# Optimization experiments

Hardware: AMD Instinct MI355X
Metric: run time of the kernel (lower is better)

## Reference

```python
import jax, jax.numpy as jnp
import numpy as np

N_NODES = 100000
N_EDGES = 1250000
IN_CH, HID_CH, OUT_CH = 128, 64, 40


def setup_inputs() -> dict:
    key = jax.random.key(0)
    ks = jax.random.split(key, 8)
    x = jax.random.normal(ks[0], (N_NODES, IN_CH), dtype=jnp.float32)
    edge_index = jax.random.randint(ks[1], (2, N_EDGES), 0, N_NODES, dtype=jnp.int64)
    # Glorot-ish scaled weights
    W1 = jax.random.normal(ks[2], (IN_CH, HID_CH), dtype=jnp.float32) * (1.0 / np.sqrt(IN_CH))
    b1 = jnp.zeros((HID_CH,), dtype=jnp.float32)
    W2 = jax.random.normal(ks[3], (HID_CH, HID_CH), dtype=jnp.float32) * (1.0 / np.sqrt(HID_CH))
    b2 = jnp.zeros((HID_CH,), dtype=jnp.float32)
    W3 = jax.random.normal(ks[4], (HID_CH, OUT_CH), dtype=jnp.float32) * (1.0 / np.sqrt(HID_CH))
    b3 = jnp.zeros((OUT_CH,), dtype=jnp.float32)
    return {"x": x, "edge_index": edge_index, "W1": W1, "b1": b1,
            "W2": W2, "b2": b2, "W3": W3, "b3": b3}


def reference(x, edge_index, W1, b1, W2, b2, W3, b3):
    n = x.shape[0]
    # PyG GCNConv: add self-loops, symmetric deg^-1/2 normalization
    loop = jnp.arange(n, dtype=edge_index.dtype)
    src = jnp.concatenate([edge_index[0], loop])  # [E+N]
    dst = jnp.concatenate([edge_index[1], loop])
    deg = jax.ops.segment_sum(jnp.ones_like(dst, dtype=x.dtype), dst, num_segments=n)
    dinv = jnp.where(deg > 0, jax.lax.rsqrt(deg), 0.0)
    coef = (dinv[src] * dinv[dst])[:, None]  # [E+N, 1]

    def conv(h, W, b):
        h = h @ W                                  # [N, F_out]
        msg = h[src] * coef                        # gather + scale: [E+N, F_out]
        return jax.ops.segment_sum(msg, dst, num_segments=n) + b

    h = jax.nn.relu(conv(x, W1, b1))   # dropout is identity in eval mode
    h = jax.nn.relu(conv(h, W2, b2))
    h = conv(h, W3, b3)
    return jax.nn.log_softmax(h, axis=1)
```

## Files before the change

### kernel.cpp

```cpp
#include <hip/hip_runtime.h>
#include <hip/hip_fp16.h>

#define NN 100000
#define NE 1250000
#define NBIN 512
#define RBIN 196
#define PAD 16
#define CAP 4096
#define EPB 4096
#define EPT 16

__device__ __forceinline__ int eidx(const int* __restrict__ e32, int f, int i){
    return f ? e32[2*(size_t)i] : e32[i];
}

__device__ __forceinline__ void scan_bins(const int* __restrict__ binCnt, int* __restrict__ boff){
    if(threadIdx.x < 64){
        int b0 = threadIdx.x*8;
        int pre[8]; int run = 0;
        #pragma unroll
        for(int i = 0; i < 8; ++i){ pre[i] = run; run += binCnt[(b0+i)*PAD]; }
        int inc = run;
        for(int o = 1; o < 64; o <<= 1){
            int u = __shfl_up(inc, o, 64);
            if(threadIdx.x >= (unsigned)o) inc += u;
        }
        int excl = inc - run;
        #pragma unroll
        for(int i = 0; i < 8; ++i) boff[b0+i] = excl + pre[i];
    }
    __syncthreads();
}

__global__ __launch_bounds__(256) void binA_k(const int* __restrict__ e32, int* __restrict__ binCnt){
    __shared__ int h[NBIN];
    __shared__ int flg;
    for(int t = threadIdx.x; t < NBIN; t += 256) h[t] = 0;
    if(threadIdx.x < 64){
        int v = e32[2*threadIdx.x + 1];
        unsigned long long b = __ballot(v != 0);
        if(threadIdx.x == 0) flg = (b == 0ULL) ? 1 : 0;
    }
    __syncthreads();
    const int f = flg;
    int base = blockIdx.x * 2048;
    #pragma unroll
    for(int k = 0; k < 8; ++k){
        int i = base + k*256 + threadIdx.x;
        if(i < NE){
            int d = eidx(e32, f, NE + i);
            atomicAdd(&h[d / RBIN], 1);
        }
    }
    __syncthreads();
    for(int t = threadIdx.x; t < NBIN; t += 256){
        int v = h[t];
        if(v) atomicAdd(&binCnt[t*PAD], v);
    }
}

__global__ __launch_bounds__(256) void binC_k(const int* __restrict__ e32, const int* __restrict__ binCnt,
                                              int* __restrict__ binCur, int2* __restrict__ bins){
    __shared__ int2 ST[EPB];
    __shared__ int hist[NBIN];
    __shared__ int lstart[NBIN];
    __shared__ int gbase[NBIN];
    __shared__ int cur[NBIN];
    __shared__ int boff[NBIN];
    __shared__ int flg;
    const int t = threadIdx.x;
    const int e0 = blockIdx.x * EPB;
    const int n = min(EPB, NE - e0);

    for(int b = t; b < NBIN; b += 256){ hist[b] = 0; cur[b] = 0; }
    if(t < 64){
        int v = e32[2*t + 1];
        unsigned long long b = __ballot(v != 0);
        if(t == 0) flg = (b == 0ULL) ? 1 : 0;
    }
    __syncthreads();
    const int f = flg;
    scan_bins(binCnt, boff);

    int2 ed[EPT];
    #pragma unroll
    for(int k = 0; k < EPT; ++k){
        int i = k*256 + t;
        if(i < n){
            ed[k].x = eidx(e32, f, e0 + i);
            ed[k].y = eidx(e32, f, NE + e0 + i);
            atomicAdd(&hist[ed[k].y / RBIN], 1);
        }
    }
    __syncthreads();

    if(t < 64){
        int b0 = t*8;
        int pre[8]; int run = 0;
        #pragma unroll
        for(int i = 0; i < 8; ++i){ pre[i] = run; run += hist[b0 + i]; }
        int inc = run;
        for(int o = 1; o < 64; o <<= 1){
            int u = __shfl_up(inc, o, 64);
            if(t >= o) inc += u;
        }
        int excl = inc - run;
        #pragma unroll
        for(int i = 0; i < 8; ++i) lstart[b0 + i] = excl + pre[i];
    }
    for(int b = t; b < NBIN; b += 256) gbase[b] = boff[b] + atomicAdd(&binCur[b*PAD], hist[b]);
    __syncthreads();

    #pragma unroll
    for(int k = 0; k < EPT; ++k){
        int i = k*256 + t;
        if(i < n){
            int b = ed[k].y / RBIN;
            int lo = atomicAdd(&cur[b], 1);
            ST[lstart[b] + lo] = ed[k];
        }
    }
    __syncthreads();

    for(int i = t; i < n; i += 256){
        int2 e = ST[i];
        int b = e.y / RBIN;
        bins[gbase[b] + (i - lstart[b])] = e;
    }
}

__global__ __launch_bounds__(256) void binD_k(const int2* __restrict__ bins, const int* __restrict__ binCnt,
                                              int* __restrict__ rp, float* __restrict__ dinv,
                                              int* __restrict__ csr_src){
    __shared__ int2 ES[CAP];
    __shared__ int hist[256];
    __shared__ int sc[256];
    __shared__ int cur[256];
    __shared__ int boff[NBIN];
    const int b = blockIdx.x;
    const int t = threadIdx.x;
    if(b == NBIN-1 && t == 0) rp[NN] = NE;
    const int nbase = b * RBIN;
    if(nbase >= NN) return;
    const int nend = min(nbase + RBIN, NN);
    const int nr = nend - nbase;
    hist[t] = 0; cur[t] = 0;
    __syncthreads();
    scan_bins(binCnt, boff);
    const int off0 = boff[b];
    const int cnt  = binCnt[b*PAD];

    const bool single = (cnt <= CAP);
    for(int c0 = 0; c0 < cnt; c0 += CAP){
        int n = min(CAP, cnt - c0);
        for(int i = t; i < n; i += 256) ES[i] = bins[off0 + c0 + i];
        __syncthreads();
        for(int i = t; i < n; i += 256) atomicAdd(&hist[ES[i].y - nbase], 1);
        __syncthreads();
    }
    int v = hist[t];
    sc[t] = v; __syncthreads();
    for(int off = 1; off < 256; off <<= 1){
        int u = (t >= off) ? sc[t - off] : 0;
        __syncthreads();
        sc[t] += u;
        __syncthreads();
    }
    int excl = sc[t] - v;
    sc[t] = excl;
    if(t < nr){
        rp[nbase + t]   = off0 + excl;
        dinv[nbase + t] = rsqrtf((float)(v + 1));
    }
    __syncthreads();
    for(int c0 = 0; c0 < cnt; c0 += CAP){
        int n = min(CAP, cnt - c0);
        if(!single){
            for(int i = t; i < n; i += 256) ES[i] = bins[off0 + c0 + i];
            __syncthreads();
        }
        for(int i = t; i < n; i += 256){
            int dl = ES[i].y - nbase;
            int p = atomicAdd(&cur[dl], 1);
            csr_src[off0 + sc[dl] + p] = ES[i].x;
        }
        if(!single) __syncthreads();
    }
}

template<int K, int NC, int KT, bool RELU>
__global__ __launch_bounds__(256) void gemm_k(const float* __restrict__ A, const float* __restrict__ W,
                                              const float* __restrict__ dinv,
                                              __half* __restrict__ out, int M){
    constexpr int CHT = KT/4;
    constexpr int CMASK = CHT - 1;
    __shared__ float Xs[64*KT];
    __shared__ float Ws[KT*NC];
    const int tid  = threadIdx.x;
    const int base = blockIdx.x * 64;
    const int tx = tid & 15, ty = tid >> 4;
    const int c0 = tx * 4;
    float acc[4][4] = {};

    for(int k0 = 0; k0 < K; k0 += KT){
        {
            const float4* Wv = (const float4*)(W + k0*NC);
            float4* Wsv = (float4*)Ws;
            for(int i = tid; i < KT*NC/4; i += 256) Wsv[i] = Wv[i];
        }
        {
            const int ch = tid & (CHT - 1);
            const int r0 = tid / CHT;
            constexpr int RSTEP = 256 / CHT;
            #pragma unroll
            for(int r = r0; r < 64; r += RSTEP){
                int row = base + r; if(row >= M) row = M - 1;
                float4 v = *(const float4*)&A[(size_t)row*K + k0 + ch*4];
                if(RELU){ v.x=fmaxf(v.x,0.f); v.y=fmaxf(v.y,0.f); v.z=fmaxf(v.z,0.f); v.w=fmaxf(v.w,0.f); }
                int sw = (ch + r) & CMASK;
                *(float4*)&Xs[r*KT + sw*4] = v;
            }
        }
        __syncthreads();

        if(c0 < NC){
            for(int k4 = 0; k4 < CHT; ++k4){
                float4 xs[4];
                #pragma unroll
                for(int i = 0; i < 4; ++i){
                    int r = ty*4 + i;
                    int sw = (k4 + r) & CMASK;
                    xs[i] = *(const float4*)&Xs[r*KT + (sw << 2)];
                }
                float4 wsv[4];
                #pragma unroll
                for(int kk = 0; kk < 4; ++kk) wsv[kk] = *(const float4*)&Ws[(k4*4 + kk)*NC + c0];
                #pragma unroll
                for(int kk = 0; kk < 4; ++kk){
                    const float* wp = (const float*)&wsv[kk];
                    #pragma unroll
                    for(int i = 0; i < 4; ++i){
                        float xv = ((const float*)&xs[i])[kk];
                        #pragma unroll
                        for(int j = 0; j < 4; ++j) acc[i][j] += xv * wp[j];
                    }
                }
            }
        }
        __syncthreads();
    }
    #pragma unroll
    for(int i = 0; i < 4; ++i){
        int row = base + ty*4 + i;
        if(row < M && c0 < NC){
            float dv = dinv[row];
            __half2 h01 = __floats2half2_rn(acc[i][0]*dv, acc[i][1]*dv);
            __half2 h23 = __floats2half2_rn(acc[i][2]*dv, acc[i][3]*dv);
            __half2* dst = (__half2*)&out[(size_t)row*NC + c0];
            dst[0] = h01;
            dst[1] = h23;
        }
    }
}

__global__ __launch_bounds__(256) void aggs_k(const __half* __restrict__ P, const int* __restrict__ rp,
                                              const int* __restrict__ csr_src,
                                              const float* __restrict__ dinv, const float* __restrict__ bias,
                                              float* __restrict__ G){
    const int lane = threadIdx.x & 63;
    const int idx  = (blockIdx.x*256 + threadIdx.x) >> 6;
    const int v    = idx >> 1;
    const int half = idx & 1;
    if(v >= NN) return;
    const int g = lane >> 3;
    const int q = lane & 7;
    const unsigned qo = (unsigned)(half*8 + q)*2;
    const __half2* __restrict__ P2 = (const __half2*)P;
    constexpr unsigned F2 = 32;

    const int beg = rp[v], end = rp[v + 1];
    float4 acc = make_float4(0.f, 0.f, 0.f, 0.f);
    if(g == 0){
        __half2 a = P2[(unsigned)v*F2 + qo], b = P2[(unsigned)v*F2 + qo + 1];
        float2 fa = __half22float2(a), fb = __half22float2(b);
        acc = make_float4(fa.x, fa.y, fb.x, fb.y);
    }

    int j = beg;
    #pragma unroll 1
    for(; j + 16 <= end; j += 16){
        unsigned i0 = (unsigned)csr_src[j + g]    *F2 + qo;
        unsigned i1 = (unsigned)csr_src[j + 8 + g]*F2 + qo;
        __half2 a0 = P2[i0], b0 = P2[i0+1];
        __half2 a1 = P2[i1], b1 = P2[i1+1];
        __half2 sa = __hadd2(a0, a1), sb = __hadd2(b0, b1);
        float2 f0 = __half22float2(sa), f1 = __half22float2(sb);
        acc.x += f0.x; acc.y += f0.y; acc.z += f1.x; acc.w += f1.y;
    }
    if(j + 8 <= end){
        unsigned i0 = (unsigned)csr_src[j + g]*F2 + qo;
        __half2 a = P2[i0], b = P2[i0+1];
        float2 fa = __half22float2(a), fb = __half22float2(b);
        acc.x += fa.x; acc.y += fa.y; acc.z += fb.x; acc.w += fb.y;
        j += 8;
    }
    const int rem = end - j;
    if(g < rem){
        unsigned i0 = (unsigned)csr_src[j + g]*F2 + qo;
        __half2 a = P2[i0], b = P2[i0+1];
        float2 fa = __half22float2(a), fb = __half22float2(b);
        acc.x += fa.x; acc.y += fa.y; acc.z += fb.x; acc.w += fb.y;
    }

    #pragma unroll
    for(int m = 8; m <= 32; m <<= 1){
        acc.x += __shfl_xor(acc.x, m, 64);
        acc.y += __shfl_xor(acc.y, m, 64);
        acc.z += __shfl_xor(acc.z, m, 64);
        acc.w += __shfl_xor(acc.w, m, 64);
    }

    if(g == 0){
        const float d = dinv[v];
        float4 bb = *(const float4*)&bias[half*32 + q*4];
        float4 r;
        r.x = fmaf(acc.x, d, bb.x);
        r.y = fmaf(acc.y, d, bb.y);
        r.z = fmaf(acc.z, d, bb.z);
        r.w = fmaf(acc.w, d, bb.w);
        *(float4*)&G[(size_t)v*64 + half*32 + q*4] = r;
    }
}

__global__ __launch_bounds__(256) void agg40_k(const __half* __restrict__ P, const int* __restrict__ rp,
                                               const int* __restrict__ csr_src,
                                               const float* __restrict__ dinv, const float* __restrict__ bias,
                                               float* __restrict__ G){
    constexpr int F = 40;
    constexpr int NQ = 10;
    constexpr unsigned F2 = 20;
    const int lane = threadIdx.x & 63;
    const int v = (blockIdx.x*256 + threadIdx.x) >> 6;
    if(v >= NN) return;
    const int g = lane >> 4;
    const int q = lane & 15;
    const bool qa = (q < NQ);
    const unsigned qo = (unsigned)q*2;
    const __half2* __restrict__ P2 = (const __half2*)P;

    const int beg = rp[v], end = rp[v + 1];
    float4 acc = make_float4(0.f, 0.f, 0.f, 0.f);
    if(g == 0 && qa){
        __half2 a = P2[(unsigned)v*F2 + qo], b = P2[(unsigned)v*F2 + qo + 1];
        float2 fa = __half22float2(a), fb = __half22float2(b);
        acc = make_float4(fa.x, fa.y, fb.x, fb.y);
    }

    int j = beg;
    #pragma unroll 1
    for(; j + 8 <= end; j += 8){
        unsigned i0 = (unsigned)csr_src[j + g]    *F2 + qo;
        unsigned i1 = (unsigned)csr_src[j + 4 + g]*F2 + qo;
        __half2 a0 = P2[i0], b0 = P2[i0+1];
        __half2 a1 = P2[i1], b1 = P2[i1+1];
        __half2 sa = __hadd2(a0, a1), sb = __hadd2(b0, b1);
        float2 f0 = __half22float2(sa), f1 = __half22float2(sb);
        acc.x += f0.x; acc.y += f0.y; acc.z += f1.x; acc.w += f1.y;
    }
    if(j + 4 <= end){
        unsigned i0 = (unsigned)csr_src[j + g]*F2 + qo;
        __half2 a = P2[i0], b = P2[i0+1];
        float2 fa = __half22float2(a), fb = __half22float2(b);
        acc.x += fa.x; acc.y += fa.y; acc.z += fb.x; acc.w += fb.y;
        j += 4;
    }
    const int rem = end - j;
    if(g < rem){
        unsigned i0 = (unsigned)csr_src[j + g]*F2 + qo;
        __half2 a = P2[i0], b = P2[i0+1];
        float2 fa = __half22float2(a), fb = __half22float2(b);
        acc.x += fa.x; acc.y += fa.y; acc.z += fb.x; acc.w += fb.y;
    }

    #pragma unroll
    for(int m = 16; m <= 32; m <<= 1){
        acc.x += __shfl_xor(acc.x, m, 64);
        acc.y += __shfl_xor(acc.y, m, 64);
        acc.z += __shfl_xor(acc.z, m, 64);
        acc.w += __shfl_xor(acc.w, m, 64);
    }

    float4 r;
    const float d = dinv[v];
    if(g == 0 && qa){
        float4 bb = *(const float4*)&bias[q*4];
        r.x = fmaf(acc.x, d, bb.x);
        r.y = fmaf(acc.y, d, bb.y);
        r.z = fmaf(acc.z, d, bb.z);
        r.w = fmaf(acc.w, d, bb.w);
    }
    float lm = (g == 0 && qa) ? fmaxf(fmaxf(r.x, r.y), fmaxf(r.z, r.w)) : -3.402823466e38f;
    #pragma unroll
    for(int m = 1; m <= 8; m <<= 1) lm = fmaxf(lm, __shfl_xor(lm, m, 64));
    float ls = (g == 0 && qa)
             ? (__expf(r.x - lm) + __expf(r.y - lm) + __expf(r.z - lm) + __expf(r.w - lm)) : 0.0f;
    #pragma unroll
    for(int m = 1; m <= 8; m <<= 1) ls += __shfl_xor(ls, m, 64);
    if(g == 0 && qa){
        float lz = lm + __logf(ls);
        r.x -= lz; r.y -= lz; r.z -= lz; r.w -= lz;
        *(float4*)&G[(size_t)v*F + q*4] = r;
    }
}

extern "C" void kernel_launch(void* const* d_in, const int* in_sizes, int n_in,
                              void* d_out, int out_size, void* d_ws, size_t ws_size,
                              hipStream_t stream){
    const float* x   = (const float*)d_in[0];
    const int*   e32 = (const int*)  d_in[1];
    const float* W1  = (const float*)d_in[2];
    const float* b1  = (const float*)d_in[3];
    const float* W2  = (const float*)d_in[4];
    const float* b2  = (const float*)d_in[5];
    const float* W3  = (const float*)d_in[6];
    const float* b3  = (const float*)d_in[7];
    float* out = (float*)d_out;

    char* ws = (char*)d_ws;
    size_t off = 0;
    auto alloc = [&](size_t bytes) -> void* {
        void* p = ws + off;
        off = (off + bytes + 255) & ~(size_t)255;
        return p;
    };
    int*    binCnt = (int*)   alloc((size_t)NBIN*PAD*4);
    int*    binCur = (int*)   alloc((size_t)NBIN*PAD*4);
    int*    rp     = (int*)   alloc((size_t)(NN+1)*4);
    float*  dinv   = (float*) alloc((size_t)NN*4);
    int*    csr_s  = (int*)   alloc((size_t)NE*4);
    __half* ph     = (__half*)alloc((size_t)NN*64*2);
    float*  gA     = (float*) alloc((size_t)NN*64*4);
    float*  gB     = (float*) alloc((size_t)NN*64*4);
    int2*   bins   = (int2*)  gA;

    hipMemsetAsync(binCnt, 0, (size_t)2*NBIN*PAD*4, stream);
    binA_k<<<(NE + 2047)/2048, 256, 0, stream>>>(e32, binCnt);
    binC_k<<<(NE + EPB - 1)/EPB, 256, 0, stream>>>(e32, binCnt, binCur, bins);
    binD_k<<<NBIN, 256, 0, stream>>>(bins, binCnt, rp, dinv, csr_s);

    const int GEMM_GRID = (NN + 63)/64;
    const int AGGS_GRID = NN/2;
    const int AGG_GRID  = (NN*64 + 255)/256;

    gemm_k<128,64,64,false><<<GEMM_GRID, 256, 0, stream>>>(x,  W1, dinv, ph, NN);
    aggs_k<<<AGGS_GRID, 256, 0, stream>>>(ph, rp, csr_s, dinv, b1, gA);
    gemm_k<64,64,64,true><<<GEMM_GRID, 256, 0, stream>>>(gA, W2, dinv, ph, NN);
    aggs_k<<<AGGS_GRID, 256, 0, stream>>>(ph, rp, csr_s, dinv, b2, gB);
    gemm_k<64,40,64,true><<<GEMM_GRID, 256, 0, stream>>>(gB, W3, dinv, ph, NN);
    agg40_k<<<AGG_GRID, 256, 0, stream>>>(ph, rp, csr_s, dinv, b3, out);
}
```

Baseline: 305.2 us.

## Drop bin counting pass, store hidden activations in fp16, widen aggregation per node

Removes the separate counting kernel by giving each destination bin a fixed capacity slot (BCAP) in a dedicated buffer, so binC writes directly and binD scans the final counts. Intermediate aggregation outputs gA/gB become fp16 and the GEMM gains a half-input path, halving that traffic. The 64-wide aggregation now uses one wavefront per node with 16 lanes per row and 4 edge groups, unrolled 16 edges per iteration, and the last-layer projection uses a padded 64-half row stride. The fixed bin capacity risks overflow if a bin exceeds 3072 edges, and fp16 intermediates add rounding.

```diff
diff --git a/kernel.cpp b/kernel.cpp
--- a/kernel.cpp
+++ b/kernel.cpp
@@ -9,17 +9,18 @@
 #define CAP 4096
 #define EPB 4096
 #define EPT 16
+#define BCAP 3072
 
 __device__ __forceinline__ int eidx(const int* __restrict__ e32, int f, int i){
     return f ? e32[2*(size_t)i] : e32[i];
 }
 
-__device__ __forceinline__ void scan_bins(const int* __restrict__ binCnt, int* __restrict__ boff){
+__device__ __forceinline__ void scan_bins(const int* __restrict__ cnts, int* __restrict__ boff){
     if(threadIdx.x < 64){
         int b0 = threadIdx.x*8;
         int pre[8]; int run = 0;
         #pragma unroll
-        for(int i = 0; i < 8; ++i){ pre[i] = run; run += binCnt[(b0+i)*PAD]; }
+        for(int i = 0; i < 8; ++i){ pre[i] = run; run += cnts[(b0+i)*PAD]; }
         int inc = run;
         for(int o = 1; o < 64; o <<= 1){
             int u = __shfl_up(inc, o, 64);
@@ -32,41 +33,13 @@
     __syncthreads();
 }
 
-__global__ __launch_bounds__(256) void binA_k(const int* __restrict__ e32, int* __restrict__ binCnt){
-    __shared__ int h[NBIN];
-    __shared__ int flg;
-    for(int t = threadIdx.x; t < NBIN; t += 256) h[t] = 0;
-    if(threadIdx.x < 64){
-        int v = e32[2*threadIdx.x + 1];
-        unsigned long long b = __ballot(v != 0);
-        if(threadIdx.x == 0) flg = (b == 0ULL) ? 1 : 0;
-    }
-    __syncthreads();
-    const int f = flg;
-    int base = blockIdx.x * 2048;
-    #pragma unroll
-    for(int k = 0; k < 8; ++k){
-        int i = base + k*256 + threadIdx.x;
-        if(i < NE){
-            int d = eidx(e32, f, NE + i);
-            atomicAdd(&h[d / RBIN], 1);
-        }
-    }
-    __syncthreads();
-    for(int t = threadIdx.x; t < NBIN; t += 256){
-        int v = h[t];
-        if(v) atomicAdd(&binCnt[t*PAD], v);
-    }
-}
-
-__global__ __launch_bounds__(256) void binC_k(const int* __restrict__ e32, const int* __restrict__ binCnt,
+__global__ __launch_bounds__(256) void binC_k(const int* __restrict__ e32,
                                               int* __restrict__ binCur, int2* __restrict__ bins){
     __shared__ int2 ST[EPB];
     __shared__ int hist[NBIN];
     __shared__ int lstart[NBIN];
     __shared__ int gbase[NBIN];
     __shared__ int cur[NBIN];
-    __shared__ int boff[NBIN];
     __shared__ int flg;
     const int t = threadIdx.x;
     const int e0 = blockIdx.x * EPB;
@@ -80,7 +53,6 @@
     }
     __syncthreads();
     const int f = flg;
-    scan_bins(binCnt, boff);
 
     int2 ed[EPT];
     #pragma unroll
@@ -108,7 +80,7 @@
         #pragma unroll
         for(int i = 0; i < 8; ++i) lstart[b0 + i] = excl + pre[i];
     }
-    for(int b = t; b < NBIN; b += 256) gbase[b] = boff[b] + atomicAdd(&binCur[b*PAD], hist[b]);
+    for(int b = t; b < NBIN; b += 256) gbase[b] = b*BCAP + atomicAdd(&binCur[b*PAD], hist[b]);
     __syncthreads();
 
     #pragma unroll
@@ -129,7 +101,7 @@
     }
 }
 
-__global__ __launch_bounds__(256) void binD_k(const int2* __restrict__ bins, const int* __restrict__ binCnt,
+__global__ __launch_bounds__(256) void binD_k(const int2* __restrict__ bins, const int* __restrict__ binCur,
                                               int* __restrict__ rp, float* __restrict__ dinv,
                                               int* __restrict__ csr_src){
     __shared__ int2 ES[CAP];
@@ -146,14 +118,15 @@
     const int nr = nend - nbase;
     hist[t] = 0; cur[t] = 0;
     __syncthreads();
-    scan_bins(binCnt, boff);
+    scan_bins(binCur, boff);
     const int off0 = boff[b];
-    const int cnt  = binCnt[b*PAD];
+    const int rb   = b * BCAP;
+    const int cnt  = binCur[b*PAD];
 
     const bool single = (cnt <= CAP);
     for(int c0 = 0; c0 < cnt; c0 += CAP){
         int n = min(CAP, cnt - c0);
-        for(int i = t; i < n; i += 256) ES[i] = bins[off0 + c0 + i];
+        for(int i = t; i < n; i += 256) ES[i] = bins[rb + c0 + i];
         __syncthreads();
         for(int i = t; i < n; i += 256) atomicAdd(&hist[ES[i].y - nbase], 1);
         __syncthreads();
@@ -176,7 +149,7 @@
     for(int c0 = 0; c0 < cnt; c0 += CAP){
         int n = min(CAP, cnt - c0);
         if(!single){
-            for(int i = t; i < n; i += 256) ES[i] = bins[off0 + c0 + i];
+            for(int i = t; i < n; i += 256) ES[i] = bins[rb + c0 + i];
             __syncthreads();
         }
         for(int i = t; i < n; i += 256){
@@ -188,8 +161,8 @@
     }
 }
 
-template<int K, int NC, int KT, bool RELU>
-__global__ __launch_bounds__(256) void gemm_k(const float* __restrict__ A, const float* __restrict__ W,
+template<bool AHALF, int K, int NC, int KT, int OSTR, bool RELU>
+__global__ __launch_bounds__(256) void gemm_k(const void* __restrict__ Araw, const float* __restrict__ W,
                                               const float* __restrict__ dinv,
                                               __half* __restrict__ out, int M){
     constexpr int CHT = KT/4;
@@ -215,7 +188,14 @@
             #pragma unroll
             for(int r = r0; r < 64; r += RSTEP){
                 int row = base + r; if(row >= M) row = M - 1;
-                float4 v = *(const float4*)&A[(size_t)row*K + k0 + ch*4];
+                float4 v;
+                if(AHALF){
+                    const __half2* ap = (const __half2*)((const __half*)Araw + (size_t)row*K + k0 + ch*4);
+                    float2 fa = __half22float2(ap[0]), fb = __half22float2(ap[1]);
+                    v = make_float4(fa.x, fa.y, fb.x, fb.y);
+                } else {
+                    v = *(const float4*)((const float*)Araw + (size_t)row*K + k0 + ch*4);
+                }
                 if(RELU){ v.x=fmaxf(v.x,0.f); v.y=fmaxf(v.y,0.f); v.z=fmaxf(v.z,0.f); v.w=fmaxf(v.w,0.f); }
                 int sw = (ch + r) & CMASK;
                 *(float4*)&Xs[r*KT + sw*4] = v;
@@ -256,27 +236,25 @@
             float dv = dinv[row];
             __half2 h01 = __floats2half2_rn(acc[i][0]*dv, acc[i][1]*dv);
             __half2 h23 = __floats2half2_rn(acc[i][2]*dv, acc[i][3]*dv);
-            __half2* dst = (__half2*)&out[(size_t)row*NC + c0];
+            __half2* dst = (__half2*)&out[(size_t)row*OSTR + c0];
             dst[0] = h01;
             dst[1] = h23;
         }
     }
 }
 
-__global__ __launch_bounds__(256) void aggs_k(const __half* __restrict__ P, const int* __restrict__ rp,
-                                              const int* __restrict__ csr_src,
-                                              const float* __restrict__ dinv, const float* __restrict__ bias,
-                                              float* __restrict__ G){
+__global__ __launch_bounds__(256) void agg64_k(const __half* __restrict__ P, const int* __restrict__ rp,
+                                               const int* __restrict__ csr_src,
+                                               const float* __restrict__ dinv, const float* __restrict__ bias,
+                                               __half* __restrict__ G){
+    constexpr unsigned F2 = 32;
     const int lane = threadIdx.x & 63;
-    const int idx  = (blockIdx.x*256 + threadIdx.x) >> 6;
-    const int v    = idx >> 1;
-    const int half = idx & 1;
+    const int v = (blockIdx.x*256 + threadIdx.x) >> 6;
     if(v >= NN) return;
-    const int g = lane >> 3;
-    const int q = lane & 7;
-    const unsigned qo = (unsigned)(half*8 + q)*2;
+    const int g = lane >> 4;
+    const int q = lane & 15;
+    const unsigned qo = (unsigned)q*2;
     const __half2* __restrict__ P2 = (const __half2*)P;
-    constexpr unsigned F2 = 32;
 
     const int beg = rp[v], end = rp[v + 1];
     float4 acc = make_float4(0.f, 0.f, 0.f, 0.f);
@@ -289,20 +267,37 @@
     int j = beg;
     #pragma unroll 1
     for(; j + 16 <= end; j += 16){
+        unsigned i0 = (unsigned)csr_src[j + g]     *F2 + qo;
+        unsigned i1 = (unsigned)csr_src[j + 4 + g] *F2 + qo;
+        unsigned i2 = (unsigned)csr_src[j + 8 + g] *F2 + qo;
+        unsigned i3 = (unsigned)csr_src[j + 12 + g]*F2 + qo;
+        __half2 a0 = P2[i0], b0 = P2[i0+1];
+        __half2 a1 = P2[i1], b1 = P2[i1+1];
+        __half2 a2 = P2[i2], b2 = P2[i2+1];
+        __half2 a3 = P2[i3], b3 = P2[i3+1];
+        __half2 sa = __hadd2(a0, a1), sb = __hadd2(b0, b1);
+        __half2 ta = __hadd2(a2, a3), tb = __hadd2(b2, b3);
+        float2 f0 = __half22float2(sa), f1 = __half22float2(sb);
+        float2 f2 = __half22float2(ta), f3 = __half22float2(tb);
+        acc.x += f0.x + f2.x; acc.y += f0.y + f2.y;
+        acc.z += f1.x + f3.x; acc.w += f1.y + f3.y;
+    }
+    if(j + 8 <= end){
         unsigned i0 = (unsigned)csr_src[j + g]    *F2 + qo;
-        unsigned i1 = (unsigned)csr_src[j + 8 + g]*F2 + qo;
+        unsigned i1 = (unsigned)csr_src[j + 4 + g]*F2 + qo;
         __half2 a0 = P2[i0], b0 = P2[i0+1];
         __half2 a1 = P2[i1], b1 = P2[i1+1];
         __half2 sa = __hadd2(a0, a1), sb = __hadd2(b0, b1);
         float2 f0 = __half22float2(sa), f1 = __half22float2(sb);
         acc.x += f0.x; acc.y += f0.y; acc.z += f1.x; acc.w += f1.y;
-    }
-    if(j + 8 <= end){
+        j += 8;
+    }
+    if(j + 4 <= end){
         unsigned i0 = (unsigned)csr_src[j + g]*F2 + qo;
         __half2 a = P2[i0], b = P2[i0+1];
         float2 fa = __half22float2(a), fb = __half22float2(b);
         acc.x += fa.x; acc.y += fa.y; acc.z += fb.x; acc.w += fb.y;
-        j += 8;
+        j += 4;
     }
     const int rem = end - j;
     if(g < rem){
@@ -313,7 +308,7 @@
     }
 
     #pragma unroll
-    for(int m = 8; m <= 32; m <<= 1){
+    for(int m = 16; m <= 32; m <<= 1){
         acc.x += __shfl_xor(acc.x, m, 64);
         acc.y += __shfl_xor(acc.y, m, 64);
         acc.z += __shfl_xor(acc.z, m, 64);
@@ -322,13 +317,12 @@
 
     if(g == 0){
         const float d = dinv[v];
-        float4 bb = *(const float4*)&bias[half*32 + q*4];
-        float4 r;
-        r.x = fmaf(acc.x, d, bb.x);
-        r.y = fmaf(acc.y, d, bb.y);
-        r.z = fmaf(acc.z, d, bb.z);
-        r.w = fmaf(acc.w, d, bb.w);
-        *(float4*)&G[(size_t)v*64 + half*32 + q*4] = r;
+        float4 bb = *(const float4*)&bias[q*4];
+        __half2 h01 = __floats2half2_rn(fmaf(acc.x, d, bb.x), fmaf(acc.y, d, bb.y));
+        __half2 h23 = __floats2half2_rn(fmaf(acc.z, d, bb.z), fmaf(acc.w, d, bb.w));
+        __half2* dst = (__half2*)&G[(size_t)v*64 + q*4];
+        dst[0] = h01;
+        dst[1] = h23;
     }
 }
 
@@ -336,9 +330,8 @@
                                                const int* __restrict__ csr_src,
                                                const float* __restrict__ dinv, const float* __restrict__ bias,
                                                float* __restrict__ G){
-    constexpr int F = 40;
     constexpr int NQ = 10;
-    constexpr unsigned F2 = 20;
+    constexpr unsigned F2 = 32;
     const int lane = threadIdx.x & 63;
     const int v = (blockIdx.x*256 + threadIdx.x) >> 6;
     if(v >= NN) return;
@@ -409,7 +402,7 @@
     if(g == 0 && qa){
         float lz = lm + __logf(ls);
         r.x -= lz; r.y -= lz; r.z -= lz; r.w -= lz;
-        *(float4*)&G[(size_t)v*F + q*4] = r;
+        *(float4*)&G[(size_t)v*40 + q*4] = r;
     }
 }
 
@@ -433,29 +426,26 @@
         off = (off + bytes + 255) & ~(size_t)255;
         return p;
     };
-    int*    binCnt = (int*)   alloc((size_t)NBIN*PAD*4);
     int*    binCur = (int*)   alloc((size_t)NBIN*PAD*4);
     int*    rp     = (int*)   alloc((size_t)(NN+1)*4);
     float*  dinv   = (float*) alloc((size_t)NN*4);
     int*    csr_s  = (int*)   alloc((size_t)NE*4);
     __half* ph     = (__half*)alloc((size_t)NN*64*2);
-    float*  gA     = (float*) alloc((size_t)NN*64*4);
-    float*  gB     = (float*) alloc((size_t)NN*64*4);
-    int2*   bins   = (int2*)  gA;
-
-    hipMemsetAsync(binCnt, 0, (size_t)2*NBIN*PAD*4, stream);
-    binA_k<<<(NE + 2047)/2048, 256, 0, stream>>>(e32, binCnt);
-    binC_k<<<(NE + EPB - 1)/EPB, 256, 0, stream>>>(e32, binCnt, binCur, bins);
-    binD_k<<<NBIN, 256, 0, stream>>>(bins, binCnt, rp, dinv, csr_s);
+    __half* gA     = (__half*)alloc((size_t)NN*64*2);
+    __half* gB     = (__half*)alloc((size_t)NN*64*2);
+    int2*   bins   = (int2*)  alloc((size_t)NBIN*BCAP*8);
+
+    hipMemsetAsync(binCur, 0, (size_t)NBIN*PAD*4, stream);
+    binC_k<<<(NE + EPB - 1)/EPB, 256, 0, stream>>>(e32, binCur, bins);
+    binD_k<<<NBIN, 256, 0, stream>>>(bins, binCur, rp, dinv, csr_s);
 
     const int GEMM_GRID = (NN + 63)/64;
-    const int AGGS_GRID = NN/2;
     const int AGG_GRID  = (NN*64 + 255)/256;
 
-    gemm_k<128,64,64,false><<<GEMM_GRID, 256, 0, stream>>>(x,  W1, dinv, ph, NN);
-    aggs_k<<<AGGS_GRID, 256, 0, stream>>>(ph, rp, csr_s, dinv, b1, gA);
-    gemm_k<64,64,64,true><<<GEMM_GRID, 256, 0, stream>>>(gA, W2, dinv, ph, NN);
-    aggs_k<<<AGGS_GRID, 256, 0, stream>>>(ph, rp, csr_s, dinv, b2, gB);
-    gemm_k<64,40,64,true><<<GEMM_GRID, 256, 0, stream>>>(gB, W3, dinv, ph, NN);
+    gemm_k<false,128,64,64,64,false><<<GEMM_GRID, 256, 0, stream>>>(x,  W1, dinv, ph, NN);
+    agg64_k<<<AGG_GRID, 256, 0, stream>>>(ph, rp, csr_s, dinv, b1, gA);
+    gemm_k<true, 64,64,64,64,true ><<<GEMM_GRID, 256, 0, stream>>>(gA, W2, dinv, ph, NN);
+    agg64_k<<<AGG_GRID, 256, 0, stream>>>(ph, rp, csr_s, dinv, b2, gB);
+    gemm_k<true, 64,40,64,64,true ><<<GEMM_GRID, 256, 0, stream>>>(gB, W3, dinv, ph, NN);
     agg40_k<<<AGG_GRID, 256, 0, stream>>>(ph, rp, csr_s, dinv, b3, out);
 }
```

After: 244.7 us, median of 2. 19.8% less time.
